# Optimization experiments

Measured on AMD Instinct MI355X. Metric: run time of the kernel, lower is better.

Reference implementation:

```python
import jax, jax.numpy as jnp
import numpy as np

EMBED_DIM = 1024
NUM_HEADS = 16
HEAD_DIM = EMBED_DIM // NUM_HEADS


def setup_inputs() -> dict:
    key = jax.random.key(0)
    ks = jax.random.split(key, 11)
    B, S, D = 4, 2048, EMBED_DIM
    s = 1.0 / np.sqrt(D)
    return {
        "q": jax.random.normal(ks[0], (B, S, D), jnp.float32),
        "k": jax.random.normal(ks[1], (B, S, D), jnp.float32),
        "v": jax.random.normal(ks[2], (B, S, D), jnp.float32),
        "Wq": jax.random.normal(ks[3], (D, D), jnp.float32) * s,
        "bq": jnp.zeros((D,), jnp.float32),
        "Wk": jax.random.normal(ks[4], (D, D), jnp.float32) * s,
        "bk": jnp.zeros((D,), jnp.float32),
        "Wv": jax.random.normal(ks[5], (D, D), jnp.float32) * s,
        "bv": jnp.zeros((D,), jnp.float32),
        "Wo": jax.random.normal(ks[6], (D, D), jnp.float32) * s,
        "bo": jnp.zeros((D,), jnp.float32),
    }


def reference(q, k, v, Wq, bq, Wk, bk, Wv, bv, Wo, bo):
    B, S, D = q.shape
    H, Hd = NUM_HEADS, HEAD_DIM
    # projections, split heads -> [B, H, S, Hd]
    qh = (q @ Wq + bq).reshape(B, S, H, Hd).transpose(0, 2, 1, 3)
    kh = (k @ Wk + bk).reshape(B, S, H, Hd).transpose(0, 2, 1, 3)
    vh = (v @ Wv + bv).reshape(B, S, H, Hd).transpose(0, 2, 1, 3)
    scale = 1.0 / jnp.sqrt(jnp.asarray(Hd, qh.dtype))
    scores = jnp.einsum('bhqd,bhkd->bhqk', qh, kh) * scale  # [B,H,S,S]
    attn = jax.nn.softmax(scores, axis=-1)  # dropout = identity in eval
    out = jnp.einsum('bhqk,bhkd->bhqd', attn, vh)
    out = out.transpose(0, 2, 1, 3).reshape(B, S, D)
    return out @ Wo + bo
```

## Files before the change

### kernel.cpp

```cpp
#include <hip/hip_runtime.h>

typedef __attribute__((ext_vector_type(8))) __bf16 bf16x8;
typedef __attribute__((ext_vector_type(4))) __bf16 bf16x4;
typedef __attribute__((ext_vector_type(4))) float f32x4;
typedef __attribute__((ext_vector_type(16))) float f32x16;
typedef __attribute__((ext_vector_type(4))) unsigned int u32x4;

#define GLDS(g, l) __builtin_amdgcn_global_load_lds( \
    (const __attribute__((address_space(1))) void*)(g), \
    (__attribute__((address_space(3))) void*)(l), 16, 0, 0)

__device__ __forceinline__ unsigned cvtpk_bf16(float lo, float hi) {
    unsigned r;
    asm("v_cvt_pk_bf16_f32 %0, %1, %2" : "=v"(r) : "v"(lo), "v"(hi));
    return r;
}
__device__ __forceinline__ void pl32swap(unsigned& a, unsigned& b) {
    asm("v_permlane32_swap_b32 %0, %1" : "+v"(a), "+v"(b));
}

__global__ __launch_bounds__(256) void cvt_tile(const float* __restrict__ q,
                                                const float* __restrict__ k,
                                                const float* __restrict__ v,
                                                __bf16* __restrict__ qo,
                                                __bf16* __restrict__ ko,
                                                __bf16* __restrict__ vo) {
    const float* src = blockIdx.z == 0 ? q : blockIdx.z == 1 ? k : v;
    __bf16* dst = blockIdx.z == 0 ? qo : blockIdx.z == 1 ? ko : vo;
    __shared__ __align__(16) __bf16 sb[128 * 64];
    const int t = threadIdx.x;
    const int m0 = blockIdx.x * 128, kk0 = blockIdx.y * 64;
    #pragma unroll
    for (int i = 0; i < 4; i++) {
        int cid = i * 256 + t;
        int r = cid >> 3, cc = cid & 7;
        const float* p = src + (size_t)(m0 + r) * 1024 + kk0 + cc * 8;
        float4 a = *(const float4*)p;
        float4 b2 = *(const float4*)(p + 4);
        bf16x8 o;
        o[0] = (__bf16)a.x;  o[1] = (__bf16)a.y;  o[2] = (__bf16)a.z;  o[3] = (__bf16)a.w;
        o[4] = (__bf16)b2.x; o[5] = (__bf16)b2.y; o[6] = (__bf16)b2.z; o[7] = (__bf16)b2.w;
        *(bf16x8*)((char*)sb + r * 128 + ((cc ^ (r & 7)) << 4)) = o;
    }
    __syncthreads();
    #pragma unroll
    for (int i = 0; i < 4; i++) {
        int cid = i * 256 + t;
        int ch = cid >> 7, r = cid & 127;
        bf16x8 o = *(const bf16x8*)((const char*)sb + r * 128 + ((ch ^ (r & 7)) << 4));
        size_t off = (((size_t)blockIdx.x * 32 + blockIdx.y * 2 + (ch >> 2)) * 4 + (ch & 3)) * 1024
                   + (size_t)r * 8;
        *(bf16x8*)(dst + off) = o;
    }
}

__global__ __launch_bounds__(256) void wtrans2(const float* __restrict__ W0,
                                               const float* __restrict__ W1,
                                               const float* __restrict__ W2,
                                               const float* __restrict__ W3,
                                               __bf16* __restrict__ O0,
                                               __bf16* __restrict__ O1,
                                               __bf16* __restrict__ O2,
                                               __bf16* __restrict__ O3) {
    const int z = blockIdx.z;
    const float* W = z == 0 ? W0 : z == 1 ? W1 : z == 2 ? W2 : W3;
    __bf16* Wt2 = z == 0 ? O0 : z == 1 ? O1 : z == 2 ? O2 : O3;
    __shared__ float lw[64][65];
    const int kt = blockIdx.y * 64, nt = blockIdx.x * 64;
    const int t = threadIdx.x;
    const int r = t >> 4;
    const int c4 = (t & 15) * 4;
    #pragma unroll
    for (int rr = 0; rr < 64; rr += 16) {
        float4 vv = *(const float4*)&W[(size_t)(kt + r + rr) * 1024 + nt + c4];
        lw[r + rr][c4 + 0] = vv.x; lw[r + rr][c4 + 1] = vv.y;
        lw[r + rr][c4 + 2] = vv.z; lw[r + rr][c4 + 3] = vv.w;
    }
    __syncthreads();
    #pragma unroll
    for (int rr = 0; rr < 64; rr += 16) {
        int n = nt + r + rr;
        bf16x4 ov;
        #pragma unroll
        for (int i = 0; i < 4; i++) ov[i] = (__bf16)lw[c4 + i][r + rr];
        int kg = kt + c4;
        size_t off = (size_t)(n >> 7) * 131072 + (size_t)(kg >> 5) * 4096
                   + (size_t)((kg >> 3) & 3) * 1024 + (size_t)(n & 127) * 8 + (kg & 7);
        *(bf16x4*)&Wt2[off] = ov;
    }
}

__global__ __launch_bounds__(256, 2)
void gemm_qkv(const __bf16* __restrict__ A0, const __bf16* __restrict__ A1,
              const __bf16* __restrict__ A2,
              const __bf16* __restrict__ B0, const __bf16* __restrict__ B1,
              const __bf16* __restrict__ B2,
              const float* __restrict__ bi0, const float* __restrict__ bi1,
              const float* __restrict__ bi2,
              void* __restrict__ C0, void* __restrict__ C1, void* __restrict__ C2) {
    __shared__ __align__(16) __bf16 sA[3 * 4096];
    __shared__ __align__(16) __bf16 sB[3 * 4096];
    const int y = blockIdx.y;
    const __bf16* At  = y == 0 ? A0 : y == 1 ? A1 : A2;
    const __bf16* Bt2 = y == 0 ? B0 : y == 1 ? B1 : B2;
    const float* bias = y == 0 ? bi0 : y == 1 ? bi1 : bi2;
    void* Cout        = y == 0 ? C0 : y == 1 ? C1 : C2;
    const int mode    = y + 1;

    const int t = threadIdx.x, l = t & 63, w = t >> 6;
    const int wr = w >> 1, wc = w & 1;
    const int bid = blockIdx.x, slot = bid >> 3;
    const int ytile = (bid & 7) * 8 + (slot & 7);
    const int xtile = slot >> 3;
    const __bf16* Ab = At + (size_t)ytile * 131072;
    const __bf16* Bb = Bt2 + (size_t)xtile * 131072;

#define GISSUE(ks_, buf_) do { \
    GLDS(Ab + (ks_) * 4096 + t * 8,        (char*)sA + (buf_) * 8192 + t * 16); \
    GLDS(Ab + (ks_) * 4096 + 2048 + t * 8, (char*)sA + (buf_) * 8192 + 4096 + t * 16); \
    GLDS(Bb + (ks_) * 4096 + t * 8,        (char*)sB + (buf_) * 8192 + t * 16); \
    GLDS(Bb + (ks_) * 4096 + 2048 + t * 8, (char*)sB + (buf_) * 8192 + 4096 + t * 16); \
} while (0)

    f32x4 acc[4][4];
    #pragma unroll
    for (int i = 0; i < 4; i++)
        #pragma unroll
        for (int j = 0; j < 4; j++) acc[i][j] = (f32x4){0.f, 0.f, 0.f, 0.f};

    GISSUE(0, 0);
    GISSUE(1, 1);
    int cur = 0;
    #pragma unroll 1
    for (int ks = 0; ks < 32; ++ks) {
        if (ks < 31) asm volatile("s_waitcnt vmcnt(4)" ::: "memory");
        else         asm volatile("s_waitcnt vmcnt(0)" ::: "memory");
        __builtin_amdgcn_s_barrier();
        __builtin_amdgcn_sched_barrier(0);
        if (ks + 2 < 32) GISSUE(ks + 2, cur >= 1 ? cur - 1 : 2);
        const __bf16* bA = sA + cur * 4096;
        const __bf16* bB = sB + cur * 4096;
        bf16x8 af[4], bfr[4];
        #pragma unroll
        for (int i = 0; i < 4; i++)
            af[i] = *(const bf16x8*)(bA + (l >> 4) * 1024 + (wr * 64 + i * 16 + (l & 15)) * 8);
        #pragma unroll
        for (int j = 0; j < 4; j++)
            bfr[j] = *(const bf16x8*)(bB + (l >> 4) * 1024 + (wc * 64 + j * 16 + (l & 15)) * 8);
        __builtin_amdgcn_s_setprio(1);
        #pragma unroll
        for (int i = 0; i < 4; i++)
            #pragma unroll
            for (int j = 0; j < 4; j++)
                acc[i][j] = __builtin_amdgcn_mfma_f32_16x16x32_bf16(af[i], bfr[j], acc[i][j], 0, 0, 0);
        __builtin_amdgcn_s_setprio(0);
        cur = cur == 2 ? 0 : cur + 1;
    }
#undef GISSUE

    const int m0 = ytile * 128, n0 = xtile * 128;
    #pragma unroll
    for (int j = 0; j < 4; j++) {
        int col = n0 + wc * 64 + j * 16 + (l & 15);
        float bv = bias[col];
        #pragma unroll
        for (int i = 0; i < 4; i++) {
            #pragma unroll
            for (int r = 0; r < 4; r++) {
                int row = m0 + wr * 64 + i * 16 + (l >> 4) * 4 + r;
                float vvv = acc[i][j][r] + bv;
                if (mode == 1) {
                    ((__bf16*)Cout)[(size_t)row * 1024 + col] = (__bf16)(vvv * 0.18033688f);
                } else if (mode == 2) {
                    int b_ = row >> 11, s_ = row & 2047, h_ = col >> 6, hd_ = col & 63;
                    size_t off = ((size_t)(b_ * 16 + h_) * 32 + (s_ >> 6)) * 4096
                               + (size_t)(hd_ >> 3) * 512 + (s_ & 63) * 8 + (hd_ & 7);
                    ((__bf16*)Cout)[off] = (__bf16)vvv;
                } else {
                    int b_ = row >> 11, s_ = row & 2047, h_ = col >> 6, d_ = col & 63;
                    size_t off = ((size_t)(b_ * 16 + h_) * 32 + (s_ >> 6)) * 4096
                               + (size_t)((s_ & 63) >> 3) * 512 + (size_t)d_ * 8 + (s_ & 7);
                    ((__bf16*)Cout)[off] = (__bf16)vvv;
                }
            }
        }
    }
}

__global__ __launch_bounds__(256, 2)
void gemm_out(const __bf16* __restrict__ At, const __bf16* __restrict__ Bt2,
              const float* __restrict__ bias, float* __restrict__ Cout) {
    __shared__ __align__(16) __bf16 sA[3 * 4096];
    __shared__ __align__(16) __bf16 sB[3 * 4096];
    const int t = threadIdx.x, l = t & 63, w = t >> 6;
    const int wr = w >> 1, wc = w & 1;
    const int bid = blockIdx.x, slot = bid >> 3;
    const int ytile = (bid & 7) * 8 + (slot & 7);
    const int xtile = slot >> 3;
    const __bf16* Ab = At + (size_t)ytile * 131072;
    const __bf16* Bb = Bt2 + (size_t)xtile * 131072;

#define GISSUE(ks_, buf_) do { \
    GLDS(Ab + (ks_) * 4096 + t * 8,        (char*)sA + (buf_) * 8192 + t * 16); \
    GLDS(Ab + (ks_) * 4096 + 2048 + t * 8, (char*)sA + (buf_) * 8192 + 4096 + t * 16); \
    GLDS(Bb + (ks_) * 4096 + t * 8,        (char*)sB + (buf_) * 8192 + t * 16); \
    GLDS(Bb + (ks_) * 4096 + 2048 + t * 8, (char*)sB + (buf_) * 8192 + 4096 + t * 16); \
} while (0)

    f32x4 acc[4][4];
    #pragma unroll
    for (int i = 0; i < 4; i++)
        #pragma unroll
        for (int j = 0; j < 4; j++) acc[i][j] = (f32x4){0.f, 0.f, 0.f, 0.f};

    GISSUE(0, 0);
    GISSUE(1, 1);
    int cur = 0;
    #pragma unroll 1
    for (int ks = 0; ks < 32; ++ks) {
        if (ks < 31) asm volatile("s_waitcnt vmcnt(4)" ::: "memory");
        else         asm volatile("s_waitcnt vmcnt(0)" ::: "memory");
        __builtin_amdgcn_s_barrier();
        __builtin_amdgcn_sched_barrier(0);
        if (ks + 2 < 32) GISSUE(ks + 2, cur >= 1 ? cur - 1 : 2);
        const __bf16* bA = sA + cur * 4096;
        const __bf16* bB = sB + cur * 4096;
        bf16x8 af[4], bfr[4];
        #pragma unroll
        for (int i = 0; i < 4; i++)
            af[i] = *(const bf16x8*)(bA + (l >> 4) * 1024 + (wr * 64 + i * 16 + (l & 15)) * 8);
        #pragma unroll
        for (int j = 0; j < 4; j++)
            bfr[j] = *(const bf16x8*)(bB + (l >> 4) * 1024 + (wc * 64 + j * 16 + (l & 15)) * 8);
        __builtin_amdgcn_s_setprio(1);
        #pragma unroll
        for (int i = 0; i < 4; i++)
            #pragma unroll
            for (int j = 0; j < 4; j++)
                acc[i][j] = __builtin_amdgcn_mfma_f32_16x16x32_bf16(af[i], bfr[j], acc[i][j], 0, 0, 0);
        __builtin_amdgcn_s_setprio(0);
        cur = cur == 2 ? 0 : cur + 1;
    }
#undef GISSUE

    const int m0 = ytile * 128, n0 = xtile * 128;
    #pragma unroll
    for (int j = 0; j < 4; j++) {
        int col = n0 + wc * 64 + j * 16 + (l & 15);
        float bv = bias[col];
        #pragma unroll
        for (int i = 0; i < 4; i++) {
            #pragma unroll
            for (int r = 0; r < 4; r++) {
                int row = m0 + wr * 64 + i * 16 + (l >> 4) * 4 + r;
                Cout[(size_t)row * 1024 + col] = acc[i][j][r] + bv;
            }
        }
    }
}

__global__ __launch_bounds__(512, 4)
void attn_fwd(const __bf16* __restrict__ Qp, const __bf16* __restrict__ Kt,
              const __bf16* __restrict__ Vtt, __bf16* __restrict__ AOt) {
    constexpr int S = 2048, D = 1024;
    __shared__ __align__(16) __bf16 sK[3 * 4096];
    __shared__ __align__(16) __bf16 sV[3 * 4096];
    __shared__ float sL[8][32];
    const int t = threadIdx.x, l = t & 63, w = t >> 6;
    const int c = l & 31, g = l >> 5;
    const int bid = blockIdx.x, slot = bid >> 3;
    const int bh = (slot >> 3) * 8 + (bid & 7);
    const int qb = slot & 7;
    const int b = bh >> 4, h = bh & 15;
    const int q0 = qb * 256;
    const __bf16* Kb = Kt + (size_t)bh * 131072;
    const __bf16* Vb = Vtt + (size_t)bh * 131072;

    bf16x8 qf[4];
    {
        const __bf16* qp = Qp + (size_t)(b * S + q0 + w * 32 + c) * D + h * 64;
        #pragma unroll
        for (int ks = 0; ks < 4; ks++)
            qf[ks] = *(const bf16x8*)(qp + ks * 16 + g * 8);
    }
    asm volatile("s_waitcnt vmcnt(0)" ::: "memory");

#define AISSUE(ti_, buf_) do { \
    GLDS(Kb + (ti_) * 4096 + t * 8, (char*)sK + (buf_) * 8192 + t * 16); \
    GLDS(Vb + (ti_) * 4096 + t * 8, (char*)sV + (buf_) * 8192 + t * 16); \
} while (0)

    f32x16 acc[2];
    acc[0] = (f32x16){}; acc[1] = (f32x16){};
    float ls = 0.f;

    AISSUE(0, 0);
    AISSUE(1, 1);
    int cur = 0;
    #pragma unroll 1
    for (int tile = 0; tile < 32; ++tile) {
        if (tile < 31) asm volatile("s_waitcnt vmcnt(2)" ::: "memory");
        else           asm volatile("s_waitcnt vmcnt(0)" ::: "memory");
        __builtin_amdgcn_s_barrier();
        __builtin_amdgcn_sched_barrier(0);
        const __bf16* bK = sK + cur * 4096;
        const __bf16* bV = sV + cur * 4096;
        #pragma unroll
        for (int kt = 0; kt < 2; kt++) {
            bf16x8 kf[4];
            #pragma unroll
            for (int ks = 0; ks < 4; ks++)
                kf[ks] = *(const bf16x8*)(bK + ((2 * ks + g) * 64 + kt * 32 + c) * 8);
            bf16x8 vq0[2], vq1[2];
            #pragma unroll
            for (int ti = 0; ti < 2; ti++) {
                vq0[ti] = *(const bf16x8*)(bV + ((4 * kt + g) * 64 + ti * 32 + c) * 8);
                vq1[ti] = *(const bf16x8*)(bV + ((4 * kt + 2 + g) * 64 + ti * 32 + c) * 8);
            }
            f32x16 St = {};
            St = __builtin_amdgcn_mfma_f32_32x32x16_bf16(kf[0], qf[0], St, 0, 0, 0);
            St = __builtin_amdgcn_mfma_f32_32x32x16_bf16(kf[1], qf[1], St, 0, 0, 0);
            St = __builtin_amdgcn_mfma_f32_32x32x16_bf16(kf[2], qf[2], St, 0, 0, 0);
            St = __builtin_amdgcn_mfma_f32_32x32x16_bf16(kf[3], qf[3], St, 0, 0, 0);
            #pragma unroll
            for (int r2 = 0; r2 < 16; r2++) {
                float p = __builtin_amdgcn_exp2f(St[r2]);
                ls += p;
                St[r2] = p;
            }
            unsigned w0 = cvtpk_bf16(St[0], St[1]),   w1 = cvtpk_bf16(St[2], St[3]);
            unsigned w2 = cvtpk_bf16(St[4], St[5]),   w3 = cvtpk_bf16(St[6], St[7]);
            unsigned w4 = cvtpk_bf16(St[8], St[9]),   w5 = cvtpk_bf16(St[10], St[11]);
            unsigned w6 = cvtpk_bf16(St[12], St[13]), w7 = cvtpk_bf16(St[14], St[15]);
            pl32swap(w0, w2); pl32swap(w1, w3);
            pl32swap(w4, w6); pl32swap(w5, w7);
            bf16x8 pa0 = __builtin_bit_cast(bf16x8, (u32x4){w0, w1, w2, w3});
            bf16x8 pa1 = __builtin_bit_cast(bf16x8, (u32x4){w4, w5, w6, w7});
            acc[0] = __builtin_amdgcn_mfma_f32_32x32x16_bf16(pa0, vq0[0], acc[0], 0, 0, 0);
            acc[1] = __builtin_amdgcn_mfma_f32_32x32x16_bf16(pa0, vq0[1], acc[1], 0, 0, 0);
            acc[0] = __builtin_amdgcn_mfma_f32_32x32x16_bf16(pa1, vq1[0], acc[0], 0, 0, 0);
            acc[1] = __builtin_amdgcn_mfma_f32_32x32x16_bf16(pa1, vq1[1], acc[1], 0, 0, 0);
        }
        if (tile + 2 < 32) AISSUE(tile + 2, cur >= 1 ? cur - 1 : 2);
        cur = cur == 2 ? 0 : cur + 1;
    }
#undef AISSUE

    float tt = ls + __shfl_xor(ls, 32);
    if (l < 32) sL[w][l] = 1.0f / tt;
    __syncthreads();

    #pragma unroll
    for (int rq = 0; rq < 4; rq++)
        #pragma unroll
        for (int rr2 = 0; rr2 < 4; rr2++) {
            int reg = rq * 4 + rr2;
            int rloc = rr2 + 8 * rq + 4 * g;
            float rn = sL[w][rloc];
            int qloc = w * 32 + rloc;
            int mt = b * 16 + qb * 2 + (qloc >> 7);
            int mr = qloc & 127;
            size_t base = ((size_t)mt * 32 + h * 2) * 4096 + (size_t)(c >> 3) * 1024
                        + (size_t)mr * 8 + (c & 7);
            AOt[base] = (__bf16)(acc[0][reg] * rn);
            AOt[base + 4096] = (__bf16)(acc[1][reg] * rn);
        }
}

extern "C" void kernel_launch(void* const* d_in, const int* in_sizes, int n_in,
                              void* d_out, int out_size, void* d_ws, size_t ws_size,
                              hipStream_t stream) {
    const float* q  = (const float*)d_in[0];
    const float* k  = (const float*)d_in[1];
    const float* v  = (const float*)d_in[2];
    const float* Wq = (const float*)d_in[3];
    const float* bq = (const float*)d_in[4];
    const float* Wk = (const float*)d_in[5];
    const float* bk = (const float*)d_in[6];
    const float* Wv = (const float*)d_in[7];
    const float* bv = (const float*)d_in[8];
    const float* Wo = (const float*)d_in[9];
    const float* bo = (const float*)d_in[10];

    char* ws = (char*)d_ws;
    const size_t MiB = 1024 * 1024;
    __bf16* Atq = (__bf16*)(ws);
    __bf16* Atk = (__bf16*)(ws + 16 * MiB);
    __bf16* Atv = (__bf16*)(ws + 32 * MiB);
    __bf16* W2q = (__bf16*)(ws + 48 * MiB);
    __bf16* W2k = (__bf16*)(ws + 50 * MiB);
    __bf16* W2v = (__bf16*)(ws + 52 * MiB);
    __bf16* W2o = (__bf16*)(ws + 54 * MiB);
    __bf16* Qp  = (__bf16*)(ws + 56 * MiB);
    __bf16* Kt  = (__bf16*)(ws + 72 * MiB);
    __bf16* Vtt = (__bf16*)(ws + 88 * MiB);
    __bf16* AOt = (__bf16*)(ws);

    cvt_tile<<<dim3(64, 16, 3), 256, 0, stream>>>(q, k, v, Atq, Atk, Atv);

    wtrans2<<<dim3(16, 16, 4), 256, 0, stream>>>(Wq, Wk, Wv, Wo, W2q, W2k, W2v, W2o);

    gemm_qkv<<<dim3(512, 3), 256, 0, stream>>>(Atq, Atk, Atv, W2q, W2k, W2v,
                                               bq, bk, bv, Qp, Kt, Vtt);

    attn_fwd<<<512, 512, 0, stream>>>(Qp, Kt, Vtt, AOt);

    gemm_out<<<512, 256, 0, stream>>>(AOt, W2o, bo, (float*)d_out);
}
```

Before: 195.6 us.

## Merge input and weight conversion kernels; stage V projection epilogue through LDS

Folds the activation conversion kernel and the weight transpose kernel into one launch, using the z grid dimension to pick the job. This removes one launch and the gap between the two kernels. The V projection epilogue (mode 3) no longer does scattered 2-byte global stores. It writes the tile into the freed shared buffers in the target layout and then issues coalesced 16-byte stores. The cost is extra LDS traffic and two barriers in that epilogue, and the merged kernel declares both shared arrays, which may lower occupancy.

Measured after the change: 188.2 us, median of 3. -3.8%, faster.

```diff
diff --git a/kernel.cpp b/kernel.cpp
--- a/kernel.cpp
+++ b/kernel.cpp
@@ -19,74 +19,75 @@
     asm("v_permlane32_swap_b32 %0, %1" : "+v"(a), "+v"(b));
 }
 
-__global__ __launch_bounds__(256) void cvt_tile(const float* __restrict__ q,
-                                                const float* __restrict__ k,
-                                                const float* __restrict__ v,
-                                                __bf16* __restrict__ qo,
-                                                __bf16* __restrict__ ko,
-                                                __bf16* __restrict__ vo) {
-    const float* src = blockIdx.z == 0 ? q : blockIdx.z == 1 ? k : v;
-    __bf16* dst = blockIdx.z == 0 ? qo : blockIdx.z == 1 ? ko : vo;
+__global__ __launch_bounds__(256) void cvtw(const float* __restrict__ q,
+                                            const float* __restrict__ k,
+                                            const float* __restrict__ v,
+                                            __bf16* __restrict__ qo,
+                                            __bf16* __restrict__ ko,
+                                            __bf16* __restrict__ vo,
+                                            const float* __restrict__ Wq,
+                                            const float* __restrict__ Wk,
+                                            const float* __restrict__ Wv,
+                                            const float* __restrict__ Wo,
+                                            __bf16* __restrict__ Oq,
+                                            __bf16* __restrict__ Ok,
+                                            __bf16* __restrict__ Ov,
+                                            __bf16* __restrict__ Oo) {
     __shared__ __align__(16) __bf16 sb[128 * 64];
+    __shared__ float lw[64][65];
     const int t = threadIdx.x;
-    const int m0 = blockIdx.x * 128, kk0 = blockIdx.y * 64;
-    #pragma unroll
-    for (int i = 0; i < 4; i++) {
-        int cid = i * 256 + t;
-        int r = cid >> 3, cc = cid & 7;
-        const float* p = src + (size_t)(m0 + r) * 1024 + kk0 + cc * 8;
-        float4 a = *(const float4*)p;
-        float4 b2 = *(const float4*)(p + 4);
-        bf16x8 o;
-        o[0] = (__bf16)a.x;  o[1] = (__bf16)a.y;  o[2] = (__bf16)a.z;  o[3] = (__bf16)a.w;
-        o[4] = (__bf16)b2.x; o[5] = (__bf16)b2.y; o[6] = (__bf16)b2.z; o[7] = (__bf16)b2.w;
-        *(bf16x8*)((char*)sb + r * 128 + ((cc ^ (r & 7)) << 4)) = o;
-    }
-    __syncthreads();
-    #pragma unroll
-    for (int i = 0; i < 4; i++) {
-        int cid = i * 256 + t;
-        int ch = cid >> 7, r = cid & 127;
-        bf16x8 o = *(const bf16x8*)((const char*)sb + r * 128 + ((ch ^ (r & 7)) << 4));
-        size_t off = (((size_t)blockIdx.x * 32 + blockIdx.y * 2 + (ch >> 2)) * 4 + (ch & 3)) * 1024
-                   + (size_t)r * 8;
-        *(bf16x8*)(dst + off) = o;
-    }
-}
-
-__global__ __launch_bounds__(256) void wtrans2(const float* __restrict__ W0,
-                                               const float* __restrict__ W1,
-                                               const float* __restrict__ W2,
-                                               const float* __restrict__ W3,
-                                               __bf16* __restrict__ O0,
-                                               __bf16* __restrict__ O1,
-                                               __bf16* __restrict__ O2,
-                                               __bf16* __restrict__ O3) {
     const int z = blockIdx.z;
-    const float* W = z == 0 ? W0 : z == 1 ? W1 : z == 2 ? W2 : W3;
-    __bf16* Wt2 = z == 0 ? O0 : z == 1 ? O1 : z == 2 ? O2 : O3;
-    __shared__ float lw[64][65];
-    const int kt = blockIdx.y * 64, nt = blockIdx.x * 64;
-    const int t = threadIdx.x;
-    const int r = t >> 4;
-    const int c4 = (t & 15) * 4;
-    #pragma unroll
-    for (int rr = 0; rr < 64; rr += 16) {
-        float4 vv = *(const float4*)&W[(size_t)(kt + r + rr) * 1024 + nt + c4];
-        lw[r + rr][c4 + 0] = vv.x; lw[r + rr][c4 + 1] = vv.y;
-        lw[r + rr][c4 + 2] = vv.z; lw[r + rr][c4 + 3] = vv.w;
-    }
-    __syncthreads();
-    #pragma unroll
-    for (int rr = 0; rr < 64; rr += 16) {
-        int n = nt + r + rr;
-        bf16x4 ov;
-        #pragma unroll
-        for (int i = 0; i < 4; i++) ov[i] = (__bf16)lw[c4 + i][r + rr];
-        int kg = kt + c4;
-        size_t off = (size_t)(n >> 7) * 131072 + (size_t)(kg >> 5) * 4096
-                   + (size_t)((kg >> 3) & 3) * 1024 + (size_t)(n & 127) * 8 + (kg & 7);
-        *(bf16x4*)&Wt2[off] = ov;
+    if (z < 3) {
+        const float* src = z == 0 ? q : z == 1 ? k : v;
+        __bf16* dst = z == 0 ? qo : z == 1 ? ko : vo;
+        const int m0 = blockIdx.x * 128, kk0 = blockIdx.y * 64;
+        #pragma unroll
+        for (int i = 0; i < 4; i++) {
+            int cid = i * 256 + t;
+            int r = cid >> 3, cc = cid & 7;
+            const float* p = src + (size_t)(m0 + r) * 1024 + kk0 + cc * 8;
+            float4 a = *(const float4*)p;
+            float4 b2 = *(const float4*)(p + 4);
+            bf16x8 o;
+            o[0] = (__bf16)a.x;  o[1] = (__bf16)a.y;  o[2] = (__bf16)a.z;  o[3] = (__bf16)a.w;
+            o[4] = (__bf16)b2.x; o[5] = (__bf16)b2.y; o[6] = (__bf16)b2.z; o[7] = (__bf16)b2.w;
+            *(bf16x8*)((char*)sb + r * 128 + ((cc ^ (r & 7)) << 4)) = o;
+        }
+        __syncthreads();
+        #pragma unroll
+        for (int i = 0; i < 4; i++) {
+            int cid = i * 256 + t;
+            int ch = cid >> 7, r = cid & 127;
+            bf16x8 o = *(const bf16x8*)((const char*)sb + r * 128 + ((ch ^ (r & 7)) << 4));
+            size_t off = (((size_t)blockIdx.x * 32 + blockIdx.y * 2 + (ch >> 2)) * 4 + (ch & 3)) * 1024
+                       + (size_t)r * 8;
+            *(bf16x8*)(dst + off) = o;
+        }
+    } else {
+        const int wi = blockIdx.x >> 4;
+        const float* W = wi == 0 ? Wq : wi == 1 ? Wk : wi == 2 ? Wv : Wo;
+        __bf16* Wt2 = wi == 0 ? Oq : wi == 1 ? Ok : wi == 2 ? Ov : Oo;
+        const int kt = blockIdx.y * 64, nt = (blockIdx.x & 15) * 64;
+        const int r = t >> 4;
+        const int c4 = (t & 15) * 4;
+        #pragma unroll
+        for (int rr = 0; rr < 64; rr += 16) {
+            float4 vv = *(const float4*)&W[(size_t)(kt + r + rr) * 1024 + nt + c4];
+            lw[r + rr][c4 + 0] = vv.x; lw[r + rr][c4 + 1] = vv.y;
+            lw[r + rr][c4 + 2] = vv.z; lw[r + rr][c4 + 3] = vv.w;
+        }
+        __syncthreads();
+        #pragma unroll
+        for (int rr = 0; rr < 64; rr += 16) {
+            int n = nt + r + rr;
+            bf16x4 ov;
+            #pragma unroll
+            for (int i = 0; i < 4; i++) ov[i] = (__bf16)lw[c4 + i][r + rr];
+            int kg = kt + c4;
+            size_t off = (size_t)(n >> 7) * 131072 + (size_t)(kg >> 5) * 4096
+                       + (size_t)((kg >> 3) & 3) * 1024 + (size_t)(n & 127) * 8 + (kg & 7);
+            *(bf16x4*)&Wt2[off] = ov;
+        }
     }
 }
 
@@ -159,6 +160,42 @@
 #undef GISSUE
 
     const int m0 = ytile * 128, n0 = xtile * 128;
+    if (mode == 3) {
+        __syncthreads();
+        #pragma unroll
+        for (int j = 0; j < 4; j++) {
+            int cl = wc * 64 + j * 16 + (l & 15);
+            float bv = bias[n0 + cl];
+            int ch = cl >> 6, d_ = cl & 63;
+            #pragma unroll
+            for (int i = 0; i < 4; i++) {
+                #pragma unroll
+                for (int r = 0; r < 4; r++) {
+                    int sl_loc = wr * 64 + i * 16 + (l >> 4) * 4 + r;
+                    int lchunk = ch * 2 + (sl_loc >> 6);
+                    int s6 = sl_loc & 63;
+                    int eidx = lchunk * 4096 + (s6 >> 3) * 512 + d_ * 8 + (s6 & 7);
+                    __bf16 vb = (__bf16)(acc[i][j][r] + bv);
+                    if (lchunk < 3) sA[eidx] = vb;
+                    else            sB[eidx - 12288] = vb;
+                }
+            }
+        }
+        __syncthreads();
+        const int b_ = m0 >> 11, s0 = m0 & 2047;
+        #pragma unroll
+        for (int u = 0; u < 8; u++) {
+            int lidx = u * 256 + t;
+            int lchunk = lidx >> 9;
+            int off16 = lidx & 511;
+            bf16x8 val;
+            if (lchunk < 3) val = *(const bf16x8*)((const char*)sA + lchunk * 8192 + off16 * 16);
+            else            val = *(const bf16x8*)((const char*)sB + off16 * 16);
+            int gch = (b_ * 16 + (n0 >> 6) + (lchunk >> 1)) * 32 + (s0 >> 6) + (lchunk & 1);
+            *(bf16x8*)((__bf16*)Cout + (size_t)gch * 4096 + off16 * 8) = val;
+        }
+        return;
+    }
     #pragma unroll
     for (int j = 0; j < 4; j++) {
         int col = n0 + wc * 64 + j * 16 + (l & 15);
@@ -171,15 +208,10 @@
                 float vvv = acc[i][j][r] + bv;
                 if (mode == 1) {
                     ((__bf16*)Cout)[(size_t)row * 1024 + col] = (__bf16)(vvv * 0.18033688f);
-                } else if (mode == 2) {
+                } else {
                     int b_ = row >> 11, s_ = row & 2047, h_ = col >> 6, hd_ = col & 63;
                     size_t off = ((size_t)(b_ * 16 + h_) * 32 + (s_ >> 6)) * 4096
                                + (size_t)(hd_ >> 3) * 512 + (s_ & 63) * 8 + (hd_ & 7);
-                    ((__bf16*)Cout)[off] = (__bf16)vvv;
-                } else {
-                    int b_ = row >> 11, s_ = row & 2047, h_ = col >> 6, d_ = col & 63;
-                    size_t off = ((size_t)(b_ * 16 + h_) * 32 + (s_ >> 6)) * 4096
-                               + (size_t)((s_ & 63) >> 3) * 512 + (size_t)d_ * 8 + (s_ & 7);
                     ((__bf16*)Cout)[off] = (__bf16)vvv;
                 }
             }
@@ -396,9 +428,8 @@
     __bf16* Vtt = (__bf16*)(ws + 88 * MiB);
     __bf16* AOt = (__bf16*)(ws);
 
-    cvt_tile<<<dim3(64, 16, 3), 256, 0, stream>>>(q, k, v, Atq, Atk, Atv);
-
-    wtrans2<<<dim3(16, 16, 4), 256, 0, stream>>>(Wq, Wk, Wv, Wo, W2q, W2k, W2v, W2o);
+    cvtw<<<dim3(64, 16, 4), 256, 0, stream>>>(q, k, v, Atq, Atk, Atv,
+                                              Wq, Wk, Wv, Wo, W2q, W2k, W2v, W2o);
 
     gemm_qkv<<<dim3(512, 3), 256, 0, stream>>>(Atq, Atk, Atv, W2q, W2k, W2v,
                                                bq, bk, bv, Qp, Kt, Vtt);
```

## Fuse fp32-to-bf16 input conversion into QKV GEMM and stage V output via LDS

Applied to the files above, without the earlier changes.

Removes the separate cvt_tile kernel. The QKV GEMM now loads fp32 activations straight into swizzled LDS via global_load_lds and converts them to bf16 while building MFMA fragments. This saves a full read/write pass of the three activation tensors and one launch, at the cost of doubling LDS traffic and size for the A tile. It also rewrites the V-projection epilogue to stage results in LDS and write 16-byte coalesced chunks instead of scattered 2-byte stores.

Measured after the change: 201.3 us. 1.03x slower.

```diff
diff --git a/kernel.cpp b/kernel.cpp
--- a/kernel.cpp
+++ b/kernel.cpp
@@ -17,41 +17,6 @@
 }
 __device__ __forceinline__ void pl32swap(unsigned& a, unsigned& b) {
     asm("v_permlane32_swap_b32 %0, %1" : "+v"(a), "+v"(b));
-}
-
-__global__ __launch_bounds__(256) void cvt_tile(const float* __restrict__ q,
-                                                const float* __restrict__ k,
-                                                const float* __restrict__ v,
-                                                __bf16* __restrict__ qo,
-                                                __bf16* __restrict__ ko,
-                                                __bf16* __restrict__ vo) {
-    const float* src = blockIdx.z == 0 ? q : blockIdx.z == 1 ? k : v;
-    __bf16* dst = blockIdx.z == 0 ? qo : blockIdx.z == 1 ? ko : vo;
-    __shared__ __align__(16) __bf16 sb[128 * 64];
-    const int t = threadIdx.x;
-    const int m0 = blockIdx.x * 128, kk0 = blockIdx.y * 64;
-    #pragma unroll
-    for (int i = 0; i < 4; i++) {
-        int cid = i * 256 + t;
-        int r = cid >> 3, cc = cid & 7;
-        const float* p = src + (size_t)(m0 + r) * 1024 + kk0 + cc * 8;
-        float4 a = *(const float4*)p;
-        float4 b2 = *(const float4*)(p + 4);
-        bf16x8 o;
-        o[0] = (__bf16)a.x;  o[1] = (__bf16)a.y;  o[2] = (__bf16)a.z;  o[3] = (__bf16)a.w;
-        o[4] = (__bf16)b2.x; o[5] = (__bf16)b2.y; o[6] = (__bf16)b2.z; o[7] = (__bf16)b2.w;
-        *(bf16x8*)((char*)sb + r * 128 + ((cc ^ (r & 7)) << 4)) = o;
-    }
-    __syncthreads();
-    #pragma unroll
-    for (int i = 0; i < 4; i++) {
-        int cid = i * 256 + t;
-        int ch = cid >> 7, r = cid & 127;
-        bf16x8 o = *(const bf16x8*)((const char*)sb + r * 128 + ((ch ^ (r & 7)) << 4));
-        size_t off = (((size_t)blockIdx.x * 32 + blockIdx.y * 2 + (ch >> 2)) * 4 + (ch & 3)) * 1024
-                   + (size_t)r * 8;
-        *(bf16x8*)(dst + off) = o;
-    }
 }
 
 __global__ __launch_bounds__(256) void wtrans2(const float* __restrict__ W0,
@@ -91,17 +56,17 @@
 }
 
 __global__ __launch_bounds__(256, 2)
-void gemm_qkv(const __bf16* __restrict__ A0, const __bf16* __restrict__ A1,
-              const __bf16* __restrict__ A2,
+void gemm_qkv(const float* __restrict__ A0, const float* __restrict__ A1,
+              const float* __restrict__ A2,
               const __bf16* __restrict__ B0, const __bf16* __restrict__ B1,
               const __bf16* __restrict__ B2,
               const float* __restrict__ bi0, const float* __restrict__ bi1,
               const float* __restrict__ bi2,
               void* __restrict__ C0, void* __restrict__ C1, void* __restrict__ C2) {
-    __shared__ __align__(16) __bf16 sA[3 * 4096];
+    __shared__ __align__(16) float  sAf[3 * 4096];
     __shared__ __align__(16) __bf16 sB[3 * 4096];
     const int y = blockIdx.y;
-    const __bf16* At  = y == 0 ? A0 : y == 1 ? A1 : A2;
+    const float* A    = y == 0 ? A0 : y == 1 ? A1 : A2;
     const __bf16* Bt2 = y == 0 ? B0 : y == 1 ? B1 : B2;
     const float* bias = y == 0 ? bi0 : y == 1 ? bi1 : bi2;
     void* Cout        = y == 0 ? C0 : y == 1 ? C1 : C2;
@@ -112,12 +77,17 @@
     const int bid = blockIdx.x, slot = bid >> 3;
     const int ytile = (bid & 7) * 8 + (slot & 7);
     const int xtile = slot >> 3;
-    const __bf16* Ab = At + (size_t)ytile * 131072;
+    const float* Ab = A + (size_t)ytile * 128 * 1024;
     const __bf16* Bb = Bt2 + (size_t)xtile * 131072;
 
+    const int arow = t >> 3;
+    const int asc = ((t & 7) ^ (arow & 7)) * 4;
+
 #define GISSUE(ks_, buf_) do { \
-    GLDS(Ab + (ks_) * 4096 + t * 8,        (char*)sA + (buf_) * 8192 + t * 16); \
-    GLDS(Ab + (ks_) * 4096 + 2048 + t * 8, (char*)sA + (buf_) * 8192 + 4096 + t * 16); \
+    GLDS(Ab + (size_t)(arow +  0) * 1024 + (ks_) * 32 + asc, (char*)sAf + (buf_) * 16384 + t * 16); \
+    GLDS(Ab + (size_t)(arow + 32) * 1024 + (ks_) * 32 + asc, (char*)sAf + (buf_) * 16384 + 4096 + t * 16); \
+    GLDS(Ab + (size_t)(arow + 64) * 1024 + (ks_) * 32 + asc, (char*)sAf + (buf_) * 16384 + 8192 + t * 16); \
+    GLDS(Ab + (size_t)(arow + 96) * 1024 + (ks_) * 32 + asc, (char*)sAf + (buf_) * 16384 + 12288 + t * 16); \
     GLDS(Bb + (ks_) * 4096 + t * 8,        (char*)sB + (buf_) * 8192 + t * 16); \
     GLDS(Bb + (ks_) * 4096 + 2048 + t * 8, (char*)sB + (buf_) * 8192 + 4096 + t * 16); \
 } while (0)
@@ -133,17 +103,27 @@
     int cur = 0;
     #pragma unroll 1
     for (int ks = 0; ks < 32; ++ks) {
-        if (ks < 31) asm volatile("s_waitcnt vmcnt(4)" ::: "memory");
+        if (ks < 31) asm volatile("s_waitcnt vmcnt(6)" ::: "memory");
         else         asm volatile("s_waitcnt vmcnt(0)" ::: "memory");
         __builtin_amdgcn_s_barrier();
         __builtin_amdgcn_sched_barrier(0);
         if (ks + 2 < 32) GISSUE(ks + 2, cur >= 1 ? cur - 1 : 2);
-        const __bf16* bA = sA + cur * 4096;
+        const char* bAf = (const char*)sAf + cur * 16384;
         const __bf16* bB = sB + cur * 4096;
         bf16x8 af[4], bfr[4];
         #pragma unroll
-        for (int i = 0; i < 4; i++)
-            af[i] = *(const bf16x8*)(bA + (l >> 4) * 1024 + (wr * 64 + i * 16 + (l & 15)) * 8);
+        for (int i = 0; i < 4; i++) {
+            int row = wr * 64 + i * 16 + (l & 15);
+            int c0 = (l >> 4) * 2, s = row & 7;
+            f32x4 lo = *(const f32x4*)(bAf + row * 128 + ((c0 ^ s) << 4));
+            f32x4 hi = *(const f32x4*)(bAf + row * 128 + (((c0 + 1) ^ s) << 4));
+            bf16x8 a;
+            a[0] = (__bf16)lo[0]; a[1] = (__bf16)lo[1];
+            a[2] = (__bf16)lo[2]; a[3] = (__bf16)lo[3];
+            a[4] = (__bf16)hi[0]; a[5] = (__bf16)hi[1];
+            a[6] = (__bf16)hi[2]; a[7] = (__bf16)hi[3];
+            af[i] = a;
+        }
         #pragma unroll
         for (int j = 0; j < 4; j++)
             bfr[j] = *(const bf16x8*)(bB + (l >> 4) * 1024 + (wc * 64 + j * 16 + (l & 15)) * 8);
@@ -159,6 +139,39 @@
 #undef GISSUE
 
     const int m0 = ytile * 128, n0 = xtile * 128;
+    if (mode == 3) {
+        __syncthreads();
+        __bf16* sv = (__bf16*)sAf;
+        #pragma unroll
+        for (int j = 0; j < 4; j++) {
+            int cl = wc * 64 + j * 16 + (l & 15);
+            float bv = bias[n0 + cl];
+            int ch = cl >> 6, d_ = cl & 63;
+            #pragma unroll
+            for (int i = 0; i < 4; i++) {
+                #pragma unroll
+                for (int r = 0; r < 4; r++) {
+                    int sl_loc = wr * 64 + i * 16 + (l >> 4) * 4 + r;
+                    int lchunk = ch * 2 + (sl_loc >> 6);
+                    int s6 = sl_loc & 63;
+                    int eidx = lchunk * 4096 + (s6 >> 3) * 512 + d_ * 8 + (s6 & 7);
+                    sv[eidx] = (__bf16)(acc[i][j][r] + bv);
+                }
+            }
+        }
+        __syncthreads();
+        const int b_ = m0 >> 11, s0 = m0 & 2047;
+        #pragma unroll
+        for (int u = 0; u < 8; u++) {
+            int lidx = u * 256 + t;
+            int lchunk = lidx >> 9;
+            int off16 = lidx & 511;
+            bf16x8 val = *(const bf16x8*)(sv + (size_t)lidx * 8);
+            int gch = (b_ * 16 + (n0 >> 6) + (lchunk >> 1)) * 32 + (s0 >> 6) + (lchunk & 1);
+            *(bf16x8*)((__bf16*)Cout + (size_t)gch * 4096 + off16 * 8) = val;
+        }
+        return;
+    }
     #pragma unroll
     for (int j = 0; j < 4; j++) {
         int col = n0 + wc * 64 + j * 16 + (l & 15);
@@ -171,15 +184,10 @@
                 float vvv = acc[i][j][r] + bv;
                 if (mode == 1) {
                     ((__bf16*)Cout)[(size_t)row * 1024 + col] = (__bf16)(vvv * 0.18033688f);
-                } else if (mode == 2) {
+                } else {
                     int b_ = row >> 11, s_ = row & 2047, h_ = col >> 6, hd_ = col & 63;
                     size_t off = ((size_t)(b_ * 16 + h_) * 32 + (s_ >> 6)) * 4096
                                + (size_t)(hd_ >> 3) * 512 + (s_ & 63) * 8 + (hd_ & 7);
-                    ((__bf16*)Cout)[off] = (__bf16)vvv;
-                } else {
-                    int b_ = row >> 11, s_ = row & 2047, h_ = col >> 6, d_ = col & 63;
-                    size_t off = ((size_t)(b_ * 16 + h_) * 32 + (s_ >> 6)) * 4096
-                               + (size_t)((s_ & 63) >> 3) * 512 + (size_t)d_ * 8 + (s_ & 7);
                     ((__bf16*)Cout)[off] = (__bf16)vvv;
                 }
             }
@@ -384,9 +392,7 @@
 
     char* ws = (char*)d_ws;
     const size_t MiB = 1024 * 1024;
-    __bf16* Atq = (__bf16*)(ws);
-    __bf16* Atk = (__bf16*)(ws + 16 * MiB);
-    __bf16* Atv = (__bf16*)(ws + 32 * MiB);
+    __bf16* AOt = (__bf16*)(ws);
     __bf16* W2q = (__bf16*)(ws + 48 * MiB);
     __bf16* W2k = (__bf16*)(ws + 50 * MiB);
     __bf16* W2v = (__bf16*)(ws + 52 * MiB);
@@ -394,13 +400,10 @@
     __bf16* Qp  = (__bf16*)(ws + 56 * MiB);
     __bf16* Kt  = (__bf16*)(ws + 72 * MiB);
     __bf16* Vtt = (__bf16*)(ws + 88 * MiB);
-    __bf16* AOt = (__bf16*)(ws);
-
-    cvt_tile<<<dim3(64, 16, 3), 256, 0, stream>>>(q, k, v, Atq, Atk, Atv);
 
     wtrans2<<<dim3(16, 16, 4), 256, 0, stream>>>(Wq, Wk, Wv, Wo, W2q, W2k, W2v, W2o);
 
-    gemm_qkv<<<dim3(512, 3), 256, 0, stream>>>(Atq, Atk, Atv, W2q, W2k, W2v,
+    gemm_qkv<<<dim3(512, 3), 256, 0, stream>>>(q, k, v, W2q, W2k, W2v,
                                                bq, bk, bv, Qp, Kt, Vtt);
 
     attn_fwd<<<512, 512, 0, stream>>>(Qp, Kt, Vtt, AOt);
```

## Merge input/weight conversion kernels and switch GEMMs to 256x128 eight-wave tiles

Applied to the files above, without the earlier changes.

Fuses the activation conversion and weight transpose into a single launch using an extra grid slice. It replaces the 128x128, 4-wave GEMMs with a templated 256x128 tile kernel that uses 8 waves and K-steps of 64. Each K-step is split into two half-phases with staggered async global-to-LDS loads and extra barriers. The larger tiles raise reuse per block and halve the block count, at the cost of 144KB of LDS per block, lower occupancy, and more barriers.

Result: slower. 200.6 us (+2.6%).

```diff
diff --git a/kernel.cpp b/kernel.cpp
--- a/kernel.cpp
+++ b/kernel.cpp
@@ -19,157 +19,211 @@
     asm("v_permlane32_swap_b32 %0, %1" : "+v"(a), "+v"(b));
 }
 
-__global__ __launch_bounds__(256) void cvt_tile(const float* __restrict__ q,
-                                                const float* __restrict__ k,
-                                                const float* __restrict__ v,
-                                                __bf16* __restrict__ qo,
-                                                __bf16* __restrict__ ko,
-                                                __bf16* __restrict__ vo) {
-    const float* src = blockIdx.z == 0 ? q : blockIdx.z == 1 ? k : v;
-    __bf16* dst = blockIdx.z == 0 ? qo : blockIdx.z == 1 ? ko : vo;
+__global__ __launch_bounds__(256) void cvtw(const float* __restrict__ q,
+                                            const float* __restrict__ k,
+                                            const float* __restrict__ v,
+                                            __bf16* __restrict__ qo,
+                                            __bf16* __restrict__ ko,
+                                            __bf16* __restrict__ vo,
+                                            const float* __restrict__ Wq,
+                                            const float* __restrict__ Wk,
+                                            const float* __restrict__ Wv,
+                                            const float* __restrict__ Wo,
+                                            __bf16* __restrict__ Oq,
+                                            __bf16* __restrict__ Ok,
+                                            __bf16* __restrict__ Ov,
+                                            __bf16* __restrict__ Oo) {
     __shared__ __align__(16) __bf16 sb[128 * 64];
+    __shared__ float lw[64][65];
     const int t = threadIdx.x;
-    const int m0 = blockIdx.x * 128, kk0 = blockIdx.y * 64;
+    const int z = blockIdx.z;
+    if (z < 3) {
+        const float* src = z == 0 ? q : z == 1 ? k : v;
+        __bf16* dst = z == 0 ? qo : z == 1 ? ko : vo;
+        const int m0 = blockIdx.x * 128, kk0 = blockIdx.y * 64;
+        #pragma unroll
+        for (int i = 0; i < 4; i++) {
+            int cid = i * 256 + t;
+            int r = cid >> 3, cc = cid & 7;
+            const float* p = src + (size_t)(m0 + r) * 1024 + kk0 + cc * 8;
+            float4 a = *(const float4*)p;
+            float4 b2 = *(const float4*)(p + 4);
+            bf16x8 o;
+            o[0] = (__bf16)a.x;  o[1] = (__bf16)a.y;  o[2] = (__bf16)a.z;  o[3] = (__bf16)a.w;
+            o[4] = (__bf16)b2.x; o[5] = (__bf16)b2.y; o[6] = (__bf16)b2.z; o[7] = (__bf16)b2.w;
+            *(bf16x8*)((char*)sb + r * 128 + ((cc ^ (r & 7)) << 4)) = o;
+        }
+        __syncthreads();
+        #pragma unroll
+        for (int i = 0; i < 4; i++) {
+            int cid = i * 256 + t;
+            int ch = cid >> 7, r = cid & 127;
+            bf16x8 o = *(const bf16x8*)((const char*)sb + r * 128 + ((ch ^ (r & 7)) << 4));
+            size_t off = (((size_t)blockIdx.x * 32 + blockIdx.y * 2 + (ch >> 2)) * 4 + (ch & 3)) * 1024
+                       + (size_t)r * 8;
+            *(bf16x8*)(dst + off) = o;
+        }
+    } else {
+        const int wi = blockIdx.x >> 4;
+        const float* W = wi == 0 ? Wq : wi == 1 ? Wk : wi == 2 ? Wv : Wo;
+        __bf16* Wt2 = wi == 0 ? Oq : wi == 1 ? Ok : wi == 2 ? Ov : Oo;
+        const int kt = blockIdx.y * 64, nt = (blockIdx.x & 15) * 64;
+        const int r = t >> 4;
+        const int c4 = (t & 15) * 4;
+        #pragma unroll
+        for (int rr = 0; rr < 64; rr += 16) {
+            float4 vv = *(const float4*)&W[(size_t)(kt + r + rr) * 1024 + nt + c4];
+            lw[r + rr][c4 + 0] = vv.x; lw[r + rr][c4 + 1] = vv.y;
+            lw[r + rr][c4 + 2] = vv.z; lw[r + rr][c4 + 3] = vv.w;
+        }
+        __syncthreads();
+        #pragma unroll
+        for (int rr = 0; rr < 64; rr += 16) {
+            int n = nt + r + rr;
+            bf16x4 ov;
+            #pragma unroll
+            for (int i = 0; i < 4; i++) ov[i] = (__bf16)lw[c4 + i][r + rr];
+            int kg = kt + c4;
+            size_t off = (size_t)(n >> 7) * 131072 + (size_t)(kg >> 5) * 4096
+                       + (size_t)((kg >> 3) & 3) * 1024 + (size_t)(n & 127) * 8 + (kg & 7);
+            *(bf16x4*)&Wt2[off] = ov;
+        }
+    }
+}
+
+template <int QKV>
+__global__ __launch_bounds__(512, 2)
+void gemm8p(const __bf16* __restrict__ A0, const __bf16* __restrict__ A1,
+            const __bf16* __restrict__ A2,
+            const __bf16* __restrict__ B0, const __bf16* __restrict__ B1,
+            const __bf16* __restrict__ B2,
+            const float* __restrict__ bi0, const float* __restrict__ bi1,
+            const float* __restrict__ bi2,
+            void* __restrict__ C0, void* __restrict__ C1, void* __restrict__ C2) {
+    __shared__ __align__(16) char S[3 * 49152];
+    const int y = blockIdx.y;
+    const __bf16* At  = QKV ? (y == 0 ? A0 : y == 1 ? A1 : A2) : A0;
+    const __bf16* Bt2 = QKV ? (y == 0 ? B0 : y == 1 ? B1 : B2) : B0;
+    const float* bias = QKV ? (y == 0 ? bi0 : y == 1 ? bi1 : bi2) : bi0;
+    void* Cout        = QKV ? (y == 0 ? C0 : y == 1 ? C1 : C2) : C0;
+    const int mode    = QKV ? y + 1 : 0;
+
+    const int t = threadIdx.x, l = t & 63;
+    const int wv = t >> 6, wm = wv >> 2, wn = wv & 3;
+    const int bid = blockIdx.x;
+    const int wgid = (bid & 7) * 32 + (bid >> 3);
+    const int bm = wgid >> 3, bn = wgid & 7;
+    const __bf16* Abase = At + (size_t)(2 * bm) * 131072;
+    const __bf16* Bbase = Bt2 + (size_t)bn * 131072;
+
+    const int aoff = wm * 16384 + ((l >> 4) << 11) + ((l & 15) << 4);
+    const int boff = 32768 + ((l >> 4) << 11) + ((wn * 32 + (l & 15)) << 4);
+
+#define STGA8(T_, sd_) do { \
+    const __bf16* s0_ = Abase + (size_t)(T_) * 8192; \
+    char* d0_ = S + (sd_) * 49152; \
+    GLDS(s0_ + t * 8,                 d0_ + t * 16); \
+    GLDS(s0_ + 4096 + t * 8,          d0_ + 8192 + t * 16); \
+    GLDS(s0_ + 131072 + t * 8,        d0_ + 16384 + t * 16); \
+    GLDS(s0_ + 131072 + 4096 + t * 8, d0_ + 24576 + t * 16); \
+} while (0)
+#define STGB8(T_, sd_) do { \
+    const __bf16* s1_ = Bbase + (size_t)(T_) * 8192; \
+    char* d1_ = S + (sd_) * 49152 + 32768; \
+    GLDS(s1_ + t * 8,        d1_ + t * 16); \
+    GLDS(s1_ + 4096 + t * 8, d1_ + 8192 + t * 16); \
+} while (0)
+
+    f32x4 acc[8][2];
     #pragma unroll
-    for (int i = 0; i < 4; i++) {
-        int cid = i * 256 + t;
-        int r = cid >> 3, cc = cid & 7;
-        const float* p = src + (size_t)(m0 + r) * 1024 + kk0 + cc * 8;
-        float4 a = *(const float4*)p;
-        float4 b2 = *(const float4*)(p + 4);
-        bf16x8 o;
-        o[0] = (__bf16)a.x;  o[1] = (__bf16)a.y;  o[2] = (__bf16)a.z;  o[3] = (__bf16)a.w;
-        o[4] = (__bf16)b2.x; o[5] = (__bf16)b2.y; o[6] = (__bf16)b2.z; o[7] = (__bf16)b2.w;
-        *(bf16x8*)((char*)sb + r * 128 + ((cc ^ (r & 7)) << 4)) = o;
-    }
-    __syncthreads();
-    #pragma unroll
-    for (int i = 0; i < 4; i++) {
-        int cid = i * 256 + t;
-        int ch = cid >> 7, r = cid & 127;
-        bf16x8 o = *(const bf16x8*)((const char*)sb + r * 128 + ((ch ^ (r & 7)) << 4));
-        size_t off = (((size_t)blockIdx.x * 32 + blockIdx.y * 2 + (ch >> 2)) * 4 + (ch & 3)) * 1024
-                   + (size_t)r * 8;
-        *(bf16x8*)(dst + off) = o;
-    }
-}
-
-__global__ __launch_bounds__(256) void wtrans2(const float* __restrict__ W0,
-                                               const float* __restrict__ W1,
-                                               const float* __restrict__ W2,
-                                               const float* __restrict__ W3,
-                                               __bf16* __restrict__ O0,
-                                               __bf16* __restrict__ O1,
-                                               __bf16* __restrict__ O2,
-                                               __bf16* __restrict__ O3) {
-    const int z = blockIdx.z;
-    const float* W = z == 0 ? W0 : z == 1 ? W1 : z == 2 ? W2 : W3;
-    __bf16* Wt2 = z == 0 ? O0 : z == 1 ? O1 : z == 2 ? O2 : O3;
-    __shared__ float lw[64][65];
-    const int kt = blockIdx.y * 64, nt = blockIdx.x * 64;
-    const int t = threadIdx.x;
-    const int r = t >> 4;
-    const int c4 = (t & 15) * 4;
-    #pragma unroll
-    for (int rr = 0; rr < 64; rr += 16) {
-        float4 vv = *(const float4*)&W[(size_t)(kt + r + rr) * 1024 + nt + c4];
-        lw[r + rr][c4 + 0] = vv.x; lw[r + rr][c4 + 1] = vv.y;
-        lw[r + rr][c4 + 2] = vv.z; lw[r + rr][c4 + 3] = vv.w;
-    }
-    __syncthreads();
-    #pragma unroll
-    for (int rr = 0; rr < 64; rr += 16) {
-        int n = nt + r + rr;
-        bf16x4 ov;
-        #pragma unroll
-        for (int i = 0; i < 4; i++) ov[i] = (__bf16)lw[c4 + i][r + rr];
-        int kg = kt + c4;
-        size_t off = (size_t)(n >> 7) * 131072 + (size_t)(kg >> 5) * 4096
-                   + (size_t)((kg >> 3) & 3) * 1024 + (size_t)(n & 127) * 8 + (kg & 7);
-        *(bf16x4*)&Wt2[off] = ov;
-    }
-}
-
-__global__ __launch_bounds__(256, 2)
-void gemm_qkv(const __bf16* __restrict__ A0, const __bf16* __restrict__ A1,
-              const __bf16* __restrict__ A2,
-              const __bf16* __restrict__ B0, const __bf16* __restrict__ B1,
-              const __bf16* __restrict__ B2,
-              const float* __restrict__ bi0, const float* __restrict__ bi1,
-              const float* __restrict__ bi2,
-              void* __restrict__ C0, void* __restrict__ C1, void* __restrict__ C2) {
-    __shared__ __align__(16) __bf16 sA[3 * 4096];
-    __shared__ __align__(16) __bf16 sB[3 * 4096];
-    const int y = blockIdx.y;
-    const __bf16* At  = y == 0 ? A0 : y == 1 ? A1 : A2;
-    const __bf16* Bt2 = y == 0 ? B0 : y == 1 ? B1 : B2;
-    const float* bias = y == 0 ? bi0 : y == 1 ? bi1 : bi2;
-    void* Cout        = y == 0 ? C0 : y == 1 ? C1 : C2;
-    const int mode    = y + 1;
-
-    const int t = threadIdx.x, l = t & 63, w = t >> 6;
-    const int wr = w >> 1, wc = w & 1;
-    const int bid = blockIdx.x, slot = bid >> 3;
-    const int ytile = (bid & 7) * 8 + (slot & 7);
-    const int xtile = slot >> 3;
-    const __bf16* Ab = At + (size_t)ytile * 131072;
-    const __bf16* Bb = Bt2 + (size_t)xtile * 131072;
-
-#define GISSUE(ks_, buf_) do { \
-    GLDS(Ab + (ks_) * 4096 + t * 8,        (char*)sA + (buf_) * 8192 + t * 16); \
-    GLDS(Ab + (ks_) * 4096 + 2048 + t * 8, (char*)sA + (buf_) * 8192 + 4096 + t * 16); \
-    GLDS(Bb + (ks_) * 4096 + t * 8,        (char*)sB + (buf_) * 8192 + t * 16); \
-    GLDS(Bb + (ks_) * 4096 + 2048 + t * 8, (char*)sB + (buf_) * 8192 + 4096 + t * 16); \
-} while (0)
-
-    f32x4 acc[4][4];
-    #pragma unroll
-    for (int i = 0; i < 4; i++)
-        #pragma unroll
-        for (int j = 0; j < 4; j++) acc[i][j] = (f32x4){0.f, 0.f, 0.f, 0.f};
-
-    GISSUE(0, 0);
-    GISSUE(1, 1);
+    for (int i = 0; i < 8; i++) {
+        acc[i][0] = (f32x4){0.f, 0.f, 0.f, 0.f};
+        acc[i][1] = (f32x4){0.f, 0.f, 0.f, 0.f};
+    }
+
+    STGA8(0, 0); STGB8(0, 0);
+    STGA8(1, 1); STGB8(1, 1);
+    asm volatile("s_waitcnt vmcnt(6)" ::: "memory");
+    __builtin_amdgcn_s_barrier();
+
     int cur = 0;
     #pragma unroll 1
-    for (int ks = 0; ks < 32; ++ks) {
-        if (ks < 31) asm volatile("s_waitcnt vmcnt(4)" ::: "memory");
+    for (int g = 0; g < 16; ++g) {
+        const int nxt = cur >= 1 ? cur - 1 : 2;
+        const char* sbp = (const char*)S + cur * 49152;
+        bf16x8 af0[4][2], bf0[2][2];
+        #pragma unroll
+        for (int ii = 0; ii < 4; ii++)
+            #pragma unroll
+            for (int s = 0; s < 2; s++)
+                af0[ii][s] = *(const bf16x8*)(sbp + aoff + s * 8192 + ii * 256);
+        #pragma unroll
+        for (int j = 0; j < 2; j++)
+            #pragma unroll
+            for (int s = 0; s < 2; s++)
+                bf0[j][s] = *(const bf16x8*)(sbp + boff + s * 8192 + j * 256);
+        if (g <= 13) STGA8(g + 2, nxt);
+        __builtin_amdgcn_s_barrier();
+        asm volatile("s_waitcnt lgkmcnt(0)" ::: "memory");
+        __builtin_amdgcn_sched_barrier(0);
+        __builtin_amdgcn_s_setprio(1);
+        #pragma unroll
+        for (int s = 0; s < 2; s++)
+            #pragma unroll
+            for (int ii = 0; ii < 4; ii++)
+                #pragma unroll
+                for (int j = 0; j < 2; j++)
+                    acc[ii][j] = __builtin_amdgcn_mfma_f32_16x16x32_bf16(
+                        af0[ii][s], bf0[j][s], acc[ii][j], 0, 0, 0);
+        __builtin_amdgcn_s_setprio(0);
+        __builtin_amdgcn_s_barrier();
+        bf16x8 af1[4][2], bf1[2][2];
+        #pragma unroll
+        for (int ii = 0; ii < 4; ii++)
+            #pragma unroll
+            for (int s = 0; s < 2; s++)
+                af1[ii][s] = *(const bf16x8*)(sbp + aoff + s * 8192 + (ii + 4) * 256);
+        #pragma unroll
+        for (int j = 0; j < 2; j++)
+            #pragma unroll
+            for (int s = 0; s < 2; s++)
+                bf1[j][s] = *(const bf16x8*)(sbp + boff + s * 8192 + j * 256);
+        if (g <= 13) STGB8(g + 2, nxt);
+        if (g <= 13) asm volatile("s_waitcnt vmcnt(6)" ::: "memory");
         else         asm volatile("s_waitcnt vmcnt(0)" ::: "memory");
         __builtin_amdgcn_s_barrier();
+        asm volatile("s_waitcnt lgkmcnt(0)" ::: "memory");
         __builtin_amdgcn_sched_barrier(0);
-        if (ks + 2 < 32) GISSUE(ks + 2, cur >= 1 ? cur - 1 : 2);
-        const __bf16* bA = sA + cur * 4096;
-        const __bf16* bB = sB + cur * 4096;
-        bf16x8 af[4], bfr[4];
-        #pragma unroll
-        for (int i = 0; i < 4; i++)
-            af[i] = *(const bf16x8*)(bA + (l >> 4) * 1024 + (wr * 64 + i * 16 + (l & 15)) * 8);
-        #pragma unroll
-        for (int j = 0; j < 4; j++)
-            bfr[j] = *(const bf16x8*)(bB + (l >> 4) * 1024 + (wc * 64 + j * 16 + (l & 15)) * 8);
         __builtin_amdgcn_s_setprio(1);
         #pragma unroll
-        for (int i = 0; i < 4; i++)
-            #pragma unroll
-            for (int j = 0; j < 4; j++)
-                acc[i][j] = __builtin_amdgcn_mfma_f32_16x16x32_bf16(af[i], bfr[j], acc[i][j], 0, 0, 0);
+        for (int s = 0; s < 2; s++)
+            #pragma unroll
+            for (int ii = 0; ii < 4; ii++)
+                #pragma unroll
+                for (int j = 0; j < 2; j++)
+                    acc[ii + 4][j] = __builtin_amdgcn_mfma_f32_16x16x32_bf16(
+                        af1[ii][s], bf1[j][s], acc[ii + 4][j], 0, 0, 0);
         __builtin_amdgcn_s_setprio(0);
+        __builtin_amdgcn_s_barrier();
         cur = cur == 2 ? 0 : cur + 1;
     }
-#undef GISSUE
-
-    const int m0 = ytile * 128, n0 = xtile * 128;
+#undef STGA8
+#undef STGB8
+
+    const int m0 = bm * 256 + wm * 128, n0 = bn * 128 + wn * 32;
     #pragma unroll
-    for (int j = 0; j < 4; j++) {
-        int col = n0 + wc * 64 + j * 16 + (l & 15);
+    for (int j = 0; j < 2; j++) {
+        int col = n0 + j * 16 + (l & 15);
         float bv = bias[col];
         #pragma unroll
-        for (int i = 0; i < 4; i++) {
+        for (int ii = 0; ii < 8; ii++) {
             #pragma unroll
             for (int r = 0; r < 4; r++) {
-                int row = m0 + wr * 64 + i * 16 + (l >> 4) * 4 + r;
-                float vvv = acc[i][j][r] + bv;
-                if (mode == 1) {
+                int row = m0 + ii * 16 + (l >> 4) * 4 + r;
+                float vvv = acc[ii][j][r] + bv;
+                if (mode == 0) {
+                    ((float*)Cout)[(size_t)row * 1024 + col] = vvv;
+                } else if (mode == 1) {
                     ((__bf16*)Cout)[(size_t)row * 1024 + col] = (__bf16)(vvv * 0.18033688f);
                 } else if (mode == 2) {
                     int b_ = row >> 11, s_ = row & 2047, h_ = col >> 6, hd_ = col & 63;
@@ -182,78 +236,6 @@
                                + (size_t)((s_ & 63) >> 3) * 512 + (size_t)d_ * 8 + (s_ & 7);
                     ((__bf16*)Cout)[off] = (__bf16)vvv;
                 }
-            }
-        }
-    }
-}
-
-__global__ __launch_bounds__(256, 2)
-void gemm_out(const __bf16* __restrict__ At, const __bf16* __restrict__ Bt2,
-              const float* __restrict__ bias, float* __restrict__ Cout) {
-    __shared__ __align__(16) __bf16 sA[3 * 4096];
-    __shared__ __align__(16) __bf16 sB[3 * 4096];
-    const int t = threadIdx.x, l = t & 63, w = t >> 6;
-    const int wr = w >> 1, wc = w & 1;
-    const int bid = blockIdx.x, slot = bid >> 3;
-    const int ytile = (bid & 7) * 8 + (slot & 7);
-    const int xtile = slot >> 3;
-    const __bf16* Ab = At + (size_t)ytile * 131072;
-    const __bf16* Bb = Bt2 + (size_t)xtile * 131072;
-
-#define GISSUE(ks_, buf_) do { \
-    GLDS(Ab + (ks_) * 4096 + t * 8,        (char*)sA + (buf_) * 8192 + t * 16); \
-    GLDS(Ab + (ks_) * 4096 + 2048 + t * 8, (char*)sA + (buf_) * 8192 + 4096 + t * 16); \
-    GLDS(Bb + (ks_) * 4096 + t * 8,        (char*)sB + (buf_) * 8192 + t * 16); \
-    GLDS(Bb + (ks_) * 4096 + 2048 + t * 8, (char*)sB + (buf_) * 8192 + 4096 + t * 16); \
-} while (0)
-
-    f32x4 acc[4][4];
-    #pragma unroll
-    for (int i = 0; i < 4; i++)
-        #pragma unroll
-        for (int j = 0; j < 4; j++) acc[i][j] = (f32x4){0.f, 0.f, 0.f, 0.f};
-
-    GISSUE(0, 0);
-    GISSUE(1, 1);
-    int cur = 0;
-    #pragma unroll 1
-    for (int ks = 0; ks < 32; ++ks) {
-        if (ks < 31) asm volatile("s_waitcnt vmcnt(4)" ::: "memory");
-        else         asm volatile("s_waitcnt vmcnt(0)" ::: "memory");
-        __builtin_amdgcn_s_barrier();
-        __builtin_amdgcn_sched_barrier(0);
-        if (ks + 2 < 32) GISSUE(ks + 2, cur >= 1 ? cur - 1 : 2);
-        const __bf16* bA = sA + cur * 4096;
-        const __bf16* bB = sB + cur * 4096;
-        bf16x8 af[4], bfr[4];
-        #pragma unroll
-        for (int i = 0; i < 4; i++)
-            af[i] = *(const bf16x8*)(bA + (l >> 4) * 1024 + (wr * 64 + i * 16 + (l & 15)) * 8);
-        #pragma unroll
-        for (int j = 0; j < 4; j++)
-            bfr[j] = *(const bf16x8*)(bB + (l >> 4) * 1024 + (wc * 64 + j * 16 + (l & 15)) * 8);
-        __builtin_amdgcn_s_setprio(1);
-        #pragma unroll
-        for (int i = 0; i < 4; i++)
-            #pragma unroll
-            for (int j = 0; j < 4; j++)
-                acc[i][j] = __builtin_amdgcn_mfma_f32_16x16x32_bf16(af[i], bfr[j], acc[i][j], 0, 0, 0);
-        __builtin_amdgcn_s_setprio(0);
-        cur = cur == 2 ? 0 : cur + 1;
-    }
-#undef GISSUE
-
-    const int m0 = ytile * 128, n0 = xtile * 128;
-    #pragma unroll
-    for (int j = 0; j < 4; j++) {
-        int col = n0 + wc * 64 + j * 16 + (l & 15);
-        float bv = bias[col];
-        #pragma unroll
-        for (int i = 0; i < 4; i++) {
-            #pragma unroll
-            for (int r = 0; r < 4; r++) {
-                int row = m0 + wr * 64 + i * 16 + (l >> 4) * 4 + r;
-                Cout[(size_t)row * 1024 + col] = acc[i][j][r] + bv;
             }
         }
     }
@@ -396,14 +378,14 @@
     __bf16* Vtt = (__bf16*)(ws + 88 * MiB);
     __bf16* AOt = (__bf16*)(ws);
 
-    cvt_tile<<<dim3(64, 16, 3), 256, 0, stream>>>(q, k, v, Atq, Atk, Atv);
-
-    wtrans2<<<dim3(16, 16, 4), 256, 0, stream>>>(Wq, Wk, Wv, Wo, W2q, W2k, W2v, W2o);
-
-    gemm_qkv<<<dim3(512, 3), 256, 0, stream>>>(Atq, Atk, Atv, W2q, W2k, W2v,
-                                               bq, bk, bv, Qp, Kt, Vtt);
+    cvtw<<<dim3(64, 16, 4), 256, 0, stream>>>(q, k, v, Atq, Atk, Atv,
+                                              Wq, Wk, Wv, Wo, W2q, W2k, W2v, W2o);
+
+    gemm8p<1><<<dim3(256, 3), 512, 0, stream>>>(Atq, Atk, Atv, W2q, W2k, W2v,
+                                                bq, bk, bv, Qp, Kt, Vtt);
 
     attn_fwd<<<512, 512, 0, stream>>>(Qp, Kt, Vtt, AOt);
 
-    gemm_out<<<512, 256, 0, stream>>>(AOt, W2o, bo, (float*)d_out);
-}
+    gemm8p<0><<<dim3(256, 1), 512, 0, stream>>>(AOt, AOt, AOt, W2o, W2o, W2o,
+                                                bo, bo, bo, d_out, d_out, d_out);
+}
```
